# Optimization experiments

Hardware: AMD Instinct MI355X
Metric: run time of the kernel (lower is better)

Reference implementation:

```python
import jax, jax.numpy as jnp
import numpy as np

D_MODEL = 2048
NUM_HEADS = 16
D_K = D_MODEL // NUM_HEADS  # 128
THETA = 10000.0
BATCH = 2
SEQ = 2048


def _rope(v, pos):
    # v: [..., S, d_k], pos: [..., S] int
    half = v.shape[-1] // 2
    inv_freq = THETA ** (-(jnp.arange(half, dtype=jnp.float32) * 2.0) / v.shape[-1])
    ang = pos[..., None].astype(jnp.float32) * inv_freq  # [..., S, half]
    cos, sin = jnp.cos(ang), jnp.sin(ang)
    x1 = v[..., 0::2]
    x2 = v[..., 1::2]
    r1 = x1 * cos - x2 * sin
    r2 = x1 * sin + x2 * cos
    return jnp.stack([r1, r2], axis=-1).reshape(v.shape)


def setup_inputs() -> dict:
    key = jax.random.key(0)
    ks = jax.random.split(key, 5)
    scale = D_MODEL ** -0.5
    x = jax.random.normal(ks[0], (BATCH, SEQ, D_MODEL), dtype=jnp.float32)
    WQ = jax.random.normal(ks[1], (D_MODEL, D_MODEL), dtype=jnp.float32) * scale
    WK = jax.random.normal(ks[2], (D_MODEL, D_MODEL), dtype=jnp.float32) * scale
    WV = jax.random.normal(ks[3], (D_MODEL, D_MODEL), dtype=jnp.float32) * scale
    WO = jax.random.normal(ks[4], (D_MODEL, D_MODEL), dtype=jnp.float32) * scale
    token_positions = jnp.broadcast_to(jnp.arange(SEQ, dtype=jnp.int32), (BATCH, SEQ))
    return {"x": x, "token_positions": token_positions, "WQ": WQ, "WK": WK, "WV": WV, "WO": WO}


def reference(x, token_positions, WQ, WK, WV, WO):
    B, S, _ = x.shape
    split = lambda t: t.reshape(B, S, NUM_HEADS, D_K).transpose(0, 2, 1, 3)  # [B,H,S,d]
    Q = split(x @ WQ.T)
    K = split(x @ WK.T)
    V = split(x @ WV.T)
    pos = token_positions[:, None, :]  # broadcast over heads
    Q = _rope(Q, pos)
    K = _rope(K, pos)
    scores = jnp.einsum('bhqd,bhkd->bhqk', Q, K) / np.sqrt(D_K).astype(np.float32)
    causal = jnp.arange(S)[:, None] >= jnp.arange(S)[None, :]  # [S,S]
    scores = jnp.where(causal, scores, -jnp.inf)
    attn = jax.nn.softmax(scores, axis=-1)
    out = jnp.einsum('bhqk,bhkd->bhqd', attn, V)
    out = out.transpose(0, 2, 1, 3).reshape(B, S, D_MODEL)
    return out @ WO.T
```

## Files before the change

kernel.cpp:

```cpp
#include <hip/hip_runtime.h>

typedef unsigned short ushort;
typedef __attribute__((ext_vector_type(8))) __bf16 bf16x8;
typedef __attribute__((ext_vector_type(8))) ushort ushort8;
typedef __attribute__((ext_vector_type(4))) float f32x4;
typedef __attribute__((ext_vector_type(16))) float f32x16;
typedef __attribute__((ext_vector_type(4))) unsigned u32x4;

#define DM 2048
#define NH 16
#define DK 128
#define BATCH 2
#define SEQ 2048
#define MROWS (BATCH*SEQ)

#define GLDS16(g, l) __builtin_amdgcn_global_load_lds(                         \
    (const __attribute__((address_space(1))) void*)(g),                        \
    (__attribute__((address_space(3))) void*)(l), 16, 0, 0)

__device__ __forceinline__ ushort f2bf(float f) {
  unsigned u = __builtin_bit_cast(unsigned, f);
  u += 0x7fffu + ((u >> 16) & 1u);
  return (ushort)(u >> 16);
}

__device__ __forceinline__ unsigned cvtpk(float lo, float hi) {
  unsigned r;
  asm("v_cvt_pk_bf16_f32 %0, %1, %2" : "=v"(r) : "v"(lo), "v"(hi));
  return r;
}

__device__ __forceinline__ void pswap(unsigned& a, unsigned& b) {
#if __has_builtin(__builtin_amdgcn_permlane32_swap)
  auto r = __builtin_amdgcn_permlane32_swap(a, b, false, false);
  a = r[0];
  b = r[1];
#else
  unsigned as = (unsigned)__shfl_xor((int)a, 32), bs = (unsigned)__shfl_xor((int)b, 32);
  bool hi = (threadIdx.x & 32) != 0;
  unsigned na = hi ? bs : a;
  unsigned nb = hi ? b : as;
  a = na;
  b = nb;
#endif
}

__global__ __launch_bounds__(256) void cvt_all(const float* __restrict__ x,
                                               const float* __restrict__ w0,
                                               const float* __restrict__ w1,
                                               const float* __restrict__ w2,
                                               const float* __restrict__ w3,
                                               ushort* __restrict__ xb,
                                               ushort* __restrict__ o0,
                                               ushort* __restrict__ o1,
                                               ushort* __restrict__ o2,
                                               ushort* __restrict__ o3) {
  int b = blockIdx.x;
  const float* src;
  ushort* dst;
  int lb;
  if (b < 4096) { src = x; dst = xb; lb = b; }
  else {
    int wsel = (b - 4096) >> 11;
    lb = (b - 4096) & 2047;
    src = (wsel == 0) ? w0 : (wsel == 1) ? w1 : (wsel == 2) ? w2 : w3;
    dst = (wsel == 0) ? o0 : (wsel == 1) ? o1 : (wsel == 2) ? o2 : o3;
  }
  int i = lb * 256 + threadIdx.x;
  const float4* p = (const float4*)src;
  float4 a = p[2 * i], bq = p[2 * i + 1];
  ushort8 o;
  o[0] = f2bf(a.x); o[1] = f2bf(a.y); o[2] = f2bf(a.z); o[3] = f2bf(a.w);
  o[4] = f2bf(bq.x); o[5] = f2bf(bq.y); o[6] = f2bf(bq.z); o[7] = f2bf(bq.w);
  *(ushort8*)(dst + (size_t)8 * i) = o;
}

__global__ __launch_bounds__(512, 2) void gemmF_qkv(const ushort* __restrict__ A,
                                                    const ushort* __restrict__ W0,
                                                    const ushort* __restrict__ W1,
                                                    const ushort* __restrict__ W2,
                                                    ushort* __restrict__ Qo,
                                                    ushort* __restrict__ Ko,
                                                    ushort* __restrict__ Vt,
                                                    const int* __restrict__ tpos) {
  extern __shared__ ushort lds[];
  constexpr int NT = DM / 64;
  constexpr int BUFSZ = 8192 + 24576;
  int f = ((int)blockIdx.x & 7) * 64 + ((int)blockIdx.x >> 3);
  int row0 = (f >> 4) * 128, col0 = (f & 15) * 128;
  const ushort* Bw[3] = {W0, W1, W2};
  const int tid = threadIdx.x;
  const int wid = tid >> 6, lane = tid & 63;
  const int l15 = lane & 15, lhi = lane >> 4;
  const int wm = wid >> 2, wn = wid & 3;
  const int swz = l15 & 7;

  f32x4 acc[4][6];
  const f32x4 z4 = {0.f, 0.f, 0.f, 0.f};
#pragma unroll
  for (int mq = 0; mq < 4; ++mq)
#pragma unroll
    for (int i = 0; i < 6; ++i) acc[mq][i] = z4;

  auto stage = [&](int kt, int buf) {
    ushort* dstA = &lds[buf * BUFSZ];
    const ushort* srcA = A + (size_t)row0 * DM + kt * 64;
#pragma unroll
    for (int j = 0; j < 2; ++j) {
      int g = j * 512 + tid;
      int r = g >> 3, c = g & 7;
      GLDS16(srcA + (size_t)r * DM + ((c ^ (r & 7)) * 8),
             &dstA[(j * 512 + wid * 64) * 8]);
    }
#pragma unroll
    for (int w3 = 0; w3 < 3; ++w3) {
      ushort* dstB = &lds[buf * BUFSZ + 8192 + w3 * 8192];
      const ushort* srcB = Bw[w3] + (size_t)col0 * DM + kt * 64;
#pragma unroll
      for (int j = 0; j < 2; ++j) {
        int g = j * 512 + tid;
        int r = g >> 3, c = g & 7;
        GLDS16(srcB + (size_t)r * DM + ((c ^ (r & 7)) * 8),
               &dstB[(j * 512 + wid * 64) * 8]);
      }
    }
  };

  stage(0, 0);
  asm volatile("s_waitcnt vmcnt(0)" ::: "memory");
  asm volatile("s_barrier" ::: "memory");

  for (int t = 0; t < NT; ++t) {
    const int cb = t & 1;
    const ushort* Ab = &lds[cb * BUFSZ];
    const ushort* Bb = Ab + 8192;
    if (t + 1 < NT) stage(t + 1, cb ^ 1);
#pragma unroll
    for (int ks = 0; ks < 2; ++ks) {
      bf16x8 af[4];
#pragma unroll
      for (int mq = 0; mq < 4; ++mq) {
        int row = wm * 64 + mq * 16 + l15;
        af[mq] = *(const bf16x8*)&Ab[row * 64 + (((ks * 4 + lhi) ^ swz) * 8)];
      }
      bf16x8 bfr[6];
#pragma unroll
      for (int w3 = 0; w3 < 3; ++w3)
#pragma unroll
        for (int n = 0; n < 2; ++n) {
          int row = wn * 32 + n * 16 + l15;
          bfr[w3 * 2 + n] =
              *(const bf16x8*)&Bb[w3 * 8192 + row * 64 + (((ks * 4 + lhi) ^ swz) * 8)];
        }
      __builtin_amdgcn_s_setprio(1);
#pragma unroll
      for (int mq = 0; mq < 4; ++mq)
#pragma unroll
        for (int i = 0; i < 6; ++i)
          acc[mq][i] = __builtin_amdgcn_mfma_f32_16x16x32_bf16(af[mq], bfr[i], acc[mq][i], 0, 0, 0);
      __builtin_amdgcn_s_setprio(0);
    }
    asm volatile("s_waitcnt vmcnt(0)" ::: "memory");
    asm volatile("s_barrier" ::: "memory");
  }

  int posr[4][4];
#pragma unroll
  for (int mq = 0; mq < 4; ++mq) {
    int grow = row0 + wm * 64 + mq * 16 + lhi * 4;
#pragma unroll
    for (int j = 0; j < 4; ++j) {
      int r = grow + j;
      posr[mq][j] = tpos[(r >> 11) * SEQ + (r & (SEQ - 1))];
    }
  }
#pragma unroll
  for (int mq = 0; mq < 4; ++mq) {
    int grow = row0 + wm * 64 + mq * 16 + lhi * 4;
#pragma unroll
    for (int n = 0; n < 2; ++n) {
      int gcol = col0 + wn * 32 + n * 16 + l15;
      int h = gcol >> 7, d = gcol & (DK - 1);
      float freq = exp2f(-0.20762050593045976f * (float)(d >> 1));
      bool oddl = (d & 1) != 0;
      float sn[4], cs[4];
#pragma unroll
      for (int j = 0; j < 4; ++j) {
        float ang = (float)posr[mq][j] * freq;
        sn[j] = __sinf(ang);
        cs[j] = __cosf(ang);
      }
#pragma unroll
      for (int w3 = 0; w3 < 2; ++w3) {
        ushort* Ow = w3 ? Ko : Qo;
#pragma unroll
        for (int j = 0; j < 4; ++j) {
          int r = grow + j;
          float v = acc[mq][w3 * 2 + n][j];
          float vp = __shfl_xor(v, 1);
          float outv = oddl ? (vp * sn[j] + v * cs[j]) : (v * cs[j] - vp * sn[j]);
          int b = r >> 11, s = r & (SEQ - 1);
          Ow[((size_t)(b * NH + h) * SEQ + s) * DK + d] = f2bf(outv);
        }
      }
    }
  }

  {
    ushort* lv = &lds[0];
#pragma unroll
    for (int mq = 0; mq < 4; ++mq)
#pragma unroll
      for (int n = 0; n < 2; ++n) {
        int col = wn * 32 + n * 16 + l15;
#pragma unroll
        for (int j = 0; j < 4; ++j) {
          int rowl = wm * 64 + mq * 16 + lhi * 4 + j;
          lv[rowl * 137 + col] = f2bf(acc[mq][4 + n][j]);
        }
      }
    __syncthreads();
    int b = row0 >> 11, s0r = row0 & (SEQ - 1), h = col0 >> 7;
    ushort* vtbase = Vt + (size_t)(b * NH + h) * DK * SEQ;
#pragma unroll
    for (int cc = 0; cc < 4; ++cc) {
      int c = cc * 512 + tid;
      int d = c >> 4, sc = (c & 15) * 8;
      ushort8 o;
#pragma unroll
      for (int k = 0; k < 8; ++k) o[k] = lv[(sc + k) * 137 + d];
      *(ushort8*)&vtbase[(size_t)d * SEQ + s0r + sc] = o;
    }
  }
}

__global__ __launch_bounds__(512, 2) void gemmF_out(const ushort* __restrict__ A,
                                                    const ushort* __restrict__ Bm,
                                                    float* __restrict__ ofp) {
  extern __shared__ ushort lds[];
  constexpr int NT = DM / 64;
  constexpr int BUFSZ = 8192 + 16384;
  int xcd = (int)blockIdx.x & 7, bi = (int)blockIdx.x >> 3;
  int row0 = (((xcd >> 1) << 3) + (bi >> 2)) * 128;
  int col0 = (((xcd & 1) << 2) + (bi & 3)) * 256;
  const int tid = threadIdx.x;
  const int wid = tid >> 6, lane = tid & 63;
  const int l15 = lane & 15, lhi = lane >> 4;
  const int wm = wid >> 2, wn = wid & 3;
  const int swz = l15 & 7;

  f32x4 acc[4][4];
  const f32x4 z4 = {0.f, 0.f, 0.f, 0.f};
#pragma unroll
  for (int mq = 0; mq < 4; ++mq)
#pragma unroll
    for (int i = 0; i < 4; ++i) acc[mq][i] = z4;

  auto stage = [&](int kt, int buf) {
    ushort* dstA = &lds[buf * BUFSZ];
    const ushort* srcA = A + (size_t)row0 * DM + kt * 64;
#pragma unroll
    for (int j = 0; j < 2; ++j) {
      int g = j * 512 + tid;
      int r = g >> 3, c = g & 7;
      GLDS16(srcA + (size_t)r * DM + ((c ^ (r & 7)) * 8),
             &dstA[(j * 512 + wid * 64) * 8]);
    }
    ushort* dstB = &lds[buf * BUFSZ + 8192];
    const ushort* srcB = Bm + (size_t)col0 * DM + kt * 64;
#pragma unroll
    for (int j = 0; j < 4; ++j) {
      int g = j * 512 + tid;
      int r = g >> 3, c = g & 7;
      GLDS16(srcB + (size_t)r * DM + ((c ^ (r & 7)) * 8),
             &dstB[(j * 512 + wid * 64) * 8]);
    }
  };

  stage(0, 0);
  stage(1, 1);

  for (int t = 0; t < NT; ++t) {
    if (t + 1 < NT)
      asm volatile("s_waitcnt vmcnt(6)" ::: "memory");
    else
      asm volatile("s_waitcnt vmcnt(0)" ::: "memory");
    __builtin_amdgcn_s_barrier();

    const int cb = t & 1;
    const ushort* Ab = &lds[cb * BUFSZ];
    const ushort* Bb = Ab + 8192;
#pragma unroll
    for (int ks = 0; ks < 2; ++ks) {
      bf16x8 af[4];
#pragma unroll
      for (int mq = 0; mq < 4; ++mq) {
        int row = wm * 64 + mq * 16 + l15;
        af[mq] = *(const bf16x8*)&Ab[row * 64 + (((ks * 4 + lhi) ^ swz) * 8)];
      }
      bf16x8 bfr[4];
#pragma unroll
      for (int n = 0; n < 4; ++n) {
        int row = wn * 64 + n * 16 + l15;
        bfr[n] = *(const bf16x8*)&Bb[row * 64 + (((ks * 4 + lhi) ^ swz) * 8)];
      }
      __builtin_amdgcn_s_setprio(1);
#pragma unroll
      for (int mq = 0; mq < 4; ++mq)
#pragma unroll
        for (int n = 0; n < 4; ++n)
          acc[mq][n] = __builtin_amdgcn_mfma_f32_16x16x32_bf16(af[mq], bfr[n], acc[mq][n], 0, 0, 0);
      __builtin_amdgcn_s_setprio(0);
    }

    __builtin_amdgcn_s_barrier();
    if (t + 2 < NT) stage(t + 2, cb);
  }

#pragma unroll
  for (int mq = 0; mq < 4; ++mq) {
    int grow = row0 + wm * 64 + mq * 16 + lhi * 4;
#pragma unroll
    for (int n = 0; n < 4; ++n) {
      int gcol = col0 + wn * 64 + n * 16 + l15;
#pragma unroll
      for (int j = 0; j < 4; ++j)
        ofp[(size_t)(grow + j) * DM + gcol] = acc[mq][n][j];
    }
  }
}

__global__ __launch_bounds__(256, 2) void attn_kernel(const ushort* __restrict__ Qb,
                                                      const ushort* __restrict__ Kb,
                                                      const ushort* __restrict__ Vt,
                                                      ushort* __restrict__ attnb) {
  __shared__ ushort lds[32768];
  const int bx = blockIdx.x;
  const int u = bx & 255, hg = bx >> 8;
  const int qt = hg ? (15 - (u & 15)) : (u & 15);
  const int bh = (u >> 4) + hg * 16;
  const int tid = threadIdx.x;
  const int w = tid >> 6, lane = tid & 63;
  const int l31 = lane & 31, hi = lane >> 5;
  const int qb = qt * 128;
  const int qsb = qb + w * 32;
  const int q = qsb + l31;
  const size_t qk_base = (size_t)bh * SEQ * DK;
  const size_t v_base = (size_t)bh * DK * SEQ;
  const int nt = (qb + 128) >> 6;

  bf16x8 qf[8];
#pragma unroll
  for (int ks = 0; ks < 8; ++ks)
    qf[ks] = *(const bf16x8*)&Qb[qk_base + (size_t)q * DK + ks * 16 + hi * 8];

  f32x16 acc[4];
#pragma unroll
  for (int dt = 0; dt < 4; ++dt)
#pragma unroll
    for (int r = 0; r < 16; ++r) acc[dt][r] = 0.f;

  float m2 = -INFINITY, lsum = 0.f;
  const float cs2 = 0.08838834764831845f * 1.4426950408889634f;

  auto stage = [&](int t, int bufsel) {
    const int kb0 = t * 64;
#pragma unroll
    for (int i = 0; i < 4; ++i) {
      int g = w * 256 + i * 64 + lane;
      int row = g >> 4, c16 = g & 15;
      GLDS16(Kb + qk_base + (size_t)(kb0 + row) * DK + ((c16 ^ (row & 7)) * 8),
             &lds[bufsel * 8192 + (w * 256 + i * 64) * 8]);
    }
#pragma unroll
    for (int i = 0; i < 4; ++i) {
      int g = w * 256 + i * 64 + lane;
      int row = g >> 3, c8 = g & 7;
      GLDS16(Vt + v_base + (size_t)row * SEQ + kb0 + ((c8 ^ (row & 7)) * 8),
             &lds[16384 + bufsel * 8192 + (w * 256 + i * 64) * 8]);
    }
  };

  stage(0, 0);
  __syncthreads();
  int buf = 0;

  for (int t = 0; t < nt; ++t) {
    if (t + 1 < nt) stage(t + 1, buf ^ 1);
    const int kb0 = t * 64;
    if (kb0 <= qsb) {
      const ushort* lk = &lds[buf * 8192];
      const ushort* lv = &lds[16384 + buf * 8192];
      const int kb1 = kb0 + 32;
      const bool diag0 = (kb0 == qsb);
      const bool have1 = (kb1 <= qsb);
      const bool diag1 = (kb1 == qsb);
      const int sw = l31 & 7;

      f32x16 s0, s1;
#pragma unroll
      for (int r = 0; r < 16; ++r) { s0[r] = 0.f; s1[r] = 0.f; }
      __builtin_amdgcn_s_setprio(1);
#pragma unroll
      for (int ks = 0; ks < 8; ++ks) {
        int g = 2 * ks + hi;
        bf16x8 kf = *(const bf16x8*)&lk[(l31 * 16 + (g ^ sw)) * 8];
        s0 = __builtin_amdgcn_mfma_f32_32x32x16_bf16(kf, qf[ks], s0, 0, 0, 0);
      }
      if (have1) {
#pragma unroll
        for (int ks = 0; ks < 8; ++ks) {
          int g = 2 * ks + hi;
          bf16x8 kf = *(const bf16x8*)&lk[((32 + l31) * 16 + (g ^ sw)) * 8];
          s1 = __builtin_amdgcn_mfma_f32_32x32x16_bf16(kf, qf[ks], s1, 0, 0, 0);
        }
      }
      __builtin_amdgcn_s_setprio(0);

      float mx = -INFINITY;
#pragma unroll
      for (int r = 0; r < 16; ++r) {
        float v = s0[r] * cs2;
        if (diag0) {
          int kk = kb0 + (r & 3) + 8 * (r >> 2) + 4 * hi;
          if (kk > q) v = -INFINITY;
        }
        s0[r] = v;
        mx = fmaxf(mx, v);
      }
      if (have1) {
#pragma unroll
        for (int r = 0; r < 16; ++r) {
          float v = s1[r] * cs2;
          if (diag1) {
            int kk = kb1 + (r & 3) + 8 * (r >> 2) + 4 * hi;
            if (kk > q) v = -INFINITY;
          }
          s1[r] = v;
          mx = fmaxf(mx, v);
        }
      }
      {
        unsigned ma = __builtin_bit_cast(unsigned, mx), mb = ma;
        pswap(ma, mb);
        mx = fmaxf(__builtin_bit_cast(float, ma), __builtin_bit_cast(float, mb));
      }

      float sc = 1.f;
      if (!__all(mx <= m2 + 11.5f)) {
        float mnew = fmaxf(m2, mx);
        sc = exp2f(m2 - mnew);
        m2 = mnew;
#pragma unroll
        for (int dt = 0; dt < 4; ++dt)
#pragma unroll
          for (int r = 0; r < 16; ++r) acc[dt][r] *= sc;
      }
      float rs = 0.f;
#pragma unroll
      for (int r = 0; r < 16; ++r) {
        float p = exp2f(s0[r] - m2);
        s0[r] = p;
        rs += p;
      }
      if (have1) {
#pragma unroll
        for (int r = 0; r < 16; ++r) {
          float p = exp2f(s1[r] - m2);
          s1[r] = p;
          rs += p;
        }
      }
      {
        unsigned ra = __builtin_bit_cast(unsigned, rs), rb = ra;
        pswap(ra, rb);
        rs = __builtin_bit_cast(float, ra) + __builtin_bit_cast(float, rb);
      }
      lsum = lsum * sc + rs;

      unsigned w0[8];
#pragma unroll
      for (int i = 0; i < 8; ++i) w0[i] = cvtpk(s0[2 * i], s0[2 * i + 1]);
      pswap(w0[0], w0[2]); pswap(w0[1], w0[3]);
      pswap(w0[4], w0[6]); pswap(w0[5], w0[7]);
      u32x4 b00 = {w0[0], w0[1], w0[2], w0[3]};
      u32x4 b01 = {w0[4], w0[5], w0[6], w0[7]};
      bf16x8 pb00 = __builtin_bit_cast(bf16x8, b00);
      bf16x8 pb01 = __builtin_bit_cast(bf16x8, b01);
      bf16x8 pb10, pb11;
      if (have1) {
        unsigned w1[8];
#pragma unroll
        for (int i = 0; i < 8; ++i) w1[i] = cvtpk(s1[2 * i], s1[2 * i + 1]);
        pswap(w1[0], w1[2]); pswap(w1[1], w1[3]);
        pswap(w1[4], w1[6]); pswap(w1[5], w1[7]);
        u32x4 b10 = {w1[0], w1[1], w1[2], w1[3]};
        u32x4 b11 = {w1[4], w1[5], w1[6], w1[7]};
        pb10 = __builtin_bit_cast(bf16x8, b10);
        pb11 = __builtin_bit_cast(bf16x8, b11);
      }

      __builtin_amdgcn_s_setprio(1);
#pragma unroll
      for (int dt = 0; dt < 4; ++dt) {
        int vr = (dt * 32 + l31) * 8;
        bf16x8 vf0 = *(const bf16x8*)&lv[(vr + ((0 + hi) ^ sw)) * 8];
        bf16x8 vf1 = *(const bf16x8*)&lv[(vr + ((2 + hi) ^ sw)) * 8];
        acc[dt] = __builtin_amdgcn_mfma_f32_32x32x16_bf16(vf0, pb00, acc[dt], 0, 0, 0);
        acc[dt] = __builtin_amdgcn_mfma_f32_32x32x16_bf16(vf1, pb01, acc[dt], 0, 0, 0);
        if (have1) {
          bf16x8 vf2 = *(const bf16x8*)&lv[(vr + ((4 + hi) ^ sw)) * 8];
          bf16x8 vf3 = *(const bf16x8*)&lv[(vr + ((6 + hi) ^ sw)) * 8];
          acc[dt] = __builtin_amdgcn_mfma_f32_32x32x16_bf16(vf2, pb10, acc[dt], 0, 0, 0);
          acc[dt] = __builtin_amdgcn_mfma_f32_32x32x16_bf16(vf3, pb11, acc[dt], 0, 0, 0);
        }
      }
      __builtin_amdgcn_s_setprio(0);
    }
    __syncthreads();
    buf ^= 1;
  }

  ushort* eo = &lds[w * 32 * 136];
  float inv = 1.0f / lsum;
#pragma unroll
  for (int dt = 0; dt < 4; ++dt)
#pragma unroll
    for (int rq = 0; rq < 4; ++rq) {
      unsigned lo = cvtpk(acc[dt][4 * rq] * inv, acc[dt][4 * rq + 1] * inv);
      unsigned hh = cvtpk(acc[dt][4 * rq + 2] * inv, acc[dt][4 * rq + 3] * inv);
      uint2 pr; pr.x = lo; pr.y = hh;
      *(uint2*)&eo[l31 * 136 + dt * 32 + rq * 8 + hi * 4] = pr;
    }
  const int b = bh >> 4, h = bh & (NH - 1);
#pragma unroll
  for (int it = 0; it < 8; ++it) {
    int row = it * 4 + (lane >> 4);
    int c8 = (lane & 15) * 8;
    ushort8 v = *(const ushort8*)&eo[row * 136 + c8];
    *(ushort8*)&attnb[((size_t)b * SEQ + qsb + row) * DM + h * DK + c8] = v;
  }
}

extern "C" void kernel_launch(void* const* d_in, const int* in_sizes, int n_in,
                              void* d_out, int out_size, void* d_ws, size_t ws_size,
                              hipStream_t stream) {
  const float* x = (const float*)d_in[0];
  const int* tpos = (const int*)d_in[1];
  const float* WQ = (const float*)d_in[2];
  const float* WK = (const float*)d_in[3];
  const float* WV = (const float*)d_in[4];
  const float* WO = (const float*)d_in[5];
  float* out = (float*)d_out;
  char* ws = (char*)d_ws;

  ushort* xb  = (ushort*)(ws + 0);
  ushort* wqb = (ushort*)(ws + 16777216);
  ushort* wkb = (ushort*)(ws + 25165824);
  ushort* wvb = (ushort*)(ws + 33554432);
  ushort* wob = (ushort*)(ws + 41943040);
  ushort* Qb  = (ushort*)(ws + 50331648);
  ushort* Kb  = (ushort*)(ws + 67108864);
  ushort* Vt  = (ushort*)(ws + 83886080);
  ushort* attnb = (ushort*)(ws + 16777216);

  hipFuncSetAttribute(reinterpret_cast<const void*>(gemmF_qkv),
                      hipFuncAttributeMaxDynamicSharedMemorySize, 131072);
  hipFuncSetAttribute(reinterpret_cast<const void*>(gemmF_out),
                      hipFuncAttributeMaxDynamicSharedMemorySize, 98304);

  cvt_all<<<12288, 256, 0, stream>>>(x, WQ, WK, WV, WO, xb, wqb, wkb, wvb, wob);

  gemmF_qkv<<<512, 512, 131072, stream>>>(xb, wqb, wkb, wvb, Qb, Kb, Vt, tpos);

  attn_kernel<<<dim3(512), 256, 0, stream>>>(Qb, Kb, Vt, attnb);

  gemmF_out<<<256, 512, 98304, stream>>>(attnb, wob, out);
}
```

Before: 232.1 us.

## Halve QKV GEMM K-tile to 32 and cut LDS to raise occupancy

```diff
diff --git a/kernel.cpp b/kernel.cpp
--- a/kernel.cpp
+++ b/kernel.cpp
@@ -75,7 +75,9 @@
   *(ushort8*)(dst + (size_t)8 * i) = o;
 }
 
-__global__ __launch_bounds__(512, 2) void gemmF_qkv(const ushort* __restrict__ A,
+#define SWZ(r) (((r) ^ ((r) >> 2)) & 3)
+
+__global__ __launch_bounds__(512, 4) void gemmF_qkv(const ushort* __restrict__ A,
                                                     const ushort* __restrict__ W0,
                                                     const ushort* __restrict__ W1,
                                                     const ushort* __restrict__ W2,
@@ -84,8 +86,8 @@
                                                     ushort* __restrict__ Vt,
                                                     const int* __restrict__ tpos) {
   extern __shared__ ushort lds[];
-  constexpr int NT = DM / 64;
-  constexpr int BUFSZ = 8192 + 24576;
+  constexpr int NT = DM / 32;
+  constexpr int BUFSZ = 16384;
   int f = ((int)blockIdx.x & 7) * 64 + ((int)blockIdx.x >> 3);
   int row0 = (f >> 4) * 128, col0 = (f & 15) * 128;
   const ushort* Bw[3] = {W0, W1, W2};
@@ -93,7 +95,6 @@
   const int wid = tid >> 6, lane = tid & 63;
   const int l15 = lane & 15, lhi = lane >> 4;
   const int wm = wid >> 2, wn = wid & 3;
-  const int swz = l15 & 7;
 
   f32x4 acc[4][6];
   const f32x4 z4 = {0.f, 0.f, 0.f, 0.f};
@@ -102,28 +103,18 @@
 #pragma unroll
     for (int i = 0; i < 6; ++i) acc[mq][i] = z4;
 
+  const int sr = tid >> 2, sc = tid & 3;
+  const ushort* srcA0 = A + (size_t)(row0 + sr) * DM + ((sc ^ SWZ(sr)) * 8);
+  const ushort* srcB0[3];
+#pragma unroll
+  for (int j = 0; j < 3; ++j)
+    srcB0[j] = Bw[j] + (size_t)(col0 + sr) * DM + ((sc ^ SWZ(sr)) * 8);
+
   auto stage = [&](int kt, int buf) {
-    ushort* dstA = &lds[buf * BUFSZ];
-    const ushort* srcA = A + (size_t)row0 * DM + kt * 64;
-#pragma unroll
-    for (int j = 0; j < 2; ++j) {
-      int g = j * 512 + tid;
-      int r = g >> 3, c = g & 7;
-      GLDS16(srcA + (size_t)r * DM + ((c ^ (r & 7)) * 8),
-             &dstA[(j * 512 + wid * 64) * 8]);
-    }
-#pragma unroll
-    for (int w3 = 0; w3 < 3; ++w3) {
-      ushort* dstB = &lds[buf * BUFSZ + 8192 + w3 * 8192];
-      const ushort* srcB = Bw[w3] + (size_t)col0 * DM + kt * 64;
-#pragma unroll
-      for (int j = 0; j < 2; ++j) {
-        int g = j * 512 + tid;
-        int r = g >> 3, c = g & 7;
-        GLDS16(srcB + (size_t)r * DM + ((c ^ (r & 7)) * 8),
-               &dstB[(j * 512 + wid * 64) * 8]);
-      }
-    }
+    GLDS16(srcA0 + kt * 32, &lds[buf * BUFSZ + wid * 512]);
+#pragma unroll
+    for (int j = 0; j < 3; ++j)
+      GLDS16(srcB0[j] + kt * 32, &lds[buf * BUFSZ + 4096 + j * 4096 + wid * 512]);
   };
 
   stage(0, 0);
@@ -132,32 +123,30 @@
 
   for (int t = 0; t < NT; ++t) {
     const int cb = t & 1;
-    const ushort* Ab = &lds[cb * BUFSZ];
-    const ushort* Bb = Ab + 8192;
+    const int base = cb * BUFSZ;
     if (t + 1 < NT) stage(t + 1, cb ^ 1);
-#pragma unroll
-    for (int ks = 0; ks < 2; ++ks) {
-      bf16x8 af[4];
-#pragma unroll
-      for (int mq = 0; mq < 4; ++mq) {
-        int row = wm * 64 + mq * 16 + l15;
-        af[mq] = *(const bf16x8*)&Ab[row * 64 + (((ks * 4 + lhi) ^ swz) * 8)];
-      }
-      bf16x8 bfr[6];
-#pragma unroll
-      for (int w3 = 0; w3 < 3; ++w3)
-#pragma unroll
-        for (int n = 0; n < 2; ++n) {
-          int row = wn * 32 + n * 16 + l15;
-          bfr[w3 * 2 + n] =
-              *(const bf16x8*)&Bb[w3 * 8192 + row * 64 + (((ks * 4 + lhi) ^ swz) * 8)];
-        }
+    bf16x8 af[4];
+#pragma unroll
+    for (int mq = 0; mq < 4; ++mq) {
+      int row = wm * 64 + mq * 16 + l15;
+      af[mq] = *(const bf16x8*)&lds[base + row * 32 + ((lhi ^ SWZ(row)) * 8)];
+    }
+#pragma unroll
+    for (int w3 = 0; w3 < 3; ++w3) {
+      bf16x8 bfr[2];
+#pragma unroll
+      for (int n = 0; n < 2; ++n) {
+        int row = wn * 32 + n * 16 + l15;
+        bfr[n] = *(const bf16x8*)&lds[base + 4096 + w3 * 4096 + row * 32 +
+                                      ((lhi ^ SWZ(row)) * 8)];
+      }
       __builtin_amdgcn_s_setprio(1);
 #pragma unroll
       for (int mq = 0; mq < 4; ++mq)
 #pragma unroll
-        for (int i = 0; i < 6; ++i)
-          acc[mq][i] = __builtin_amdgcn_mfma_f32_16x16x32_bf16(af[mq], bfr[i], acc[mq][i], 0, 0, 0);
+        for (int n = 0; n < 2; ++n)
+          acc[mq][w3 * 2 + n] = __builtin_amdgcn_mfma_f32_16x16x32_bf16(
+              af[mq], bfr[n], acc[mq][w3 * 2 + n], 0, 0, 0);
       __builtin_amdgcn_s_setprio(0);
     }
     asm volatile("s_waitcnt vmcnt(0)" ::: "memory");
@@ -208,6 +197,7 @@
 
   {
     ushort* lv = &lds[0];
+    __syncthreads();
 #pragma unroll
     for (int mq = 0; mq < 4; ++mq)
 #pragma unroll
@@ -225,11 +215,11 @@
 #pragma unroll
     for (int cc = 0; cc < 4; ++cc) {
       int c = cc * 512 + tid;
-      int d = c >> 4, sc = (c & 15) * 8;
+      int d = c >> 4, scx = (c & 15) * 8;
       ushort8 o;
 #pragma unroll
-      for (int k = 0; k < 8; ++k) o[k] = lv[(sc + k) * 137 + d];
-      *(ushort8*)&vtbase[(size_t)d * SEQ + s0r + sc] = o;
+      for (int k = 0; k < 8; ++k) o[k] = lv[(scx + k) * 137 + d];
+      *(ushort8*)&vtbase[(size_t)d * SEQ + s0r + scx] = o;
     }
   }
 }
@@ -565,13 +555,13 @@
   ushort* attnb = (ushort*)(ws + 16777216);
 
   hipFuncSetAttribute(reinterpret_cast<const void*>(gemmF_qkv),
-                      hipFuncAttributeMaxDynamicSharedMemorySize, 131072);
+                      hipFuncAttributeMaxDynamicSharedMemorySize, 65536);
   hipFuncSetAttribute(reinterpret_cast<const void*>(gemmF_out),
                       hipFuncAttributeMaxDynamicSharedMemorySize, 98304);
 
   cvt_all<<<12288, 256, 0, stream>>>(x, WQ, WK, WV, WO, xb, wqb, wkb, wvb, wob);
 
-  gemmF_qkv<<<512, 512, 131072, stream>>>(xb, wqb, wkb, wvb, Qb, Kb, Vt, tpos);
+  gemmF_qkv<<<512, 512, 65536, stream>>>(xb, wqb, wkb, wvb, Qb, Kb, Vt, tpos);
 
   attn_kernel<<<dim3(512), 256, 0, stream>>>(Qb, Kb, Vt, attnb);
 
```

After: 255.6 us. +10.1%, slower.
